# Performance work log

Measured on AMD Instinct MI355X. Metric: run time of the kernel, lower is better.

Reference implementation:

```python
import jax, jax.numpy as jnp
import numpy as np

N_NODES = 100000
N_EDGES = 1600000
HID = 128
N_CONV = 3  # num_layers - 1
OUT_DIM = 1
BN_EPS = 1e-5


def _batchnorm(z, gamma, beta):
    # training-mode BN over node dim (batch statistics, biased variance)
    mean = jnp.mean(z, axis=0)
    var = jnp.mean((z - mean) ** 2, axis=0)
    return (z - mean) * jax.lax.rsqrt(var + BN_EPS) * gamma + beta


def setup_inputs() -> dict:
    key = jax.random.key(0)
    ks = jax.random.split(key, 16)
    s = 0.05
    inp = {
        "x": jax.random.randint(ks[0], (N_NODES,), 0, 2, dtype=jnp.int32),
        "edge_index": jax.random.randint(ks[1], (2, N_EDGES), 0, N_NODES, dtype=jnp.int64),
        "emb": jax.random.normal(ks[2], (2, HID), jnp.float32) * s,
        "W1": jax.random.normal(ks[3], (N_CONV, HID, HID), jnp.float32) * s,
        "W2": jax.random.normal(ks[4], (N_CONV, HID, HID), jnp.float32) * s,
        "bn1_g": jnp.ones((N_CONV, HID), jnp.float32),
        "bn1_b": jnp.zeros((N_CONV, HID), jnp.float32),
        "bn2_g": jnp.ones((N_CONV, HID), jnp.float32),
        "bn2_b": jnp.zeros((N_CONV, HID), jnp.float32),
        "rW1": jax.random.normal(ks[5], (4 * HID, HID), jnp.float32) * s,
        "rb1": jnp.zeros((HID,), jnp.float32),
        "rW2": jax.random.normal(ks[6], (HID, OUT_DIM), jnp.float32) * s,
        "rb2": jnp.zeros((OUT_DIM,), jnp.float32),
    }
    return inp


def reference(x, edge_index, emb, W1, W2, bn1_g, bn1_b, bn2_g, bn2_b, rW1, rb1, rW2, rb2):
    n = x.shape[0]
    src, dst = edge_index[0], edge_index[1]
    h = emb[x]  # [N, HID]
    reps = [h]
    for i in range(N_CONV):
        # GINConv: mlp((1+eps)*h + sum_{j in N(i)} h_j), eps=0
        agg = jax.ops.segment_sum(h[src], dst, num_segments=n)
        z = h + agg
        z = jnp.einsum('nd,df->nf', z, W1[i])
        z = jax.nn.relu(_batchnorm(z, bn1_g[i], bn1_b[i]))
        z = jnp.einsum('nd,df->nf', z, W2[i])
        z = _batchnorm(z, bn2_g[i], bn2_b[i])  # PyG BatchNorm after conv
        h = jax.nn.elu(z)
        reps.append(h)
    cat = jnp.concatenate(reps, axis=-1)  # [N, 4*HID]
    hid = jax.nn.relu(cat @ rW1 + rb1)
    return hid @ rW2 + rb2  # [N, OUT_DIM]
```

## Files before the change

### kernel.cpp

```cpp
#include <hip/hip_runtime.h>
#include <hip/hip_fp16.h>
#include <cstdint>
#include <cstddef>

#define NN 100000
#define NE 1600000
#define HID 128
#define BN_EPS 1e-5f
#define NB_SCAN 98
#define BM 96
#define NBLK ((NN + BM - 1) / BM)
#define NBC  ((NN + 255) / 256)
#define SA 72
#define SC_CHUNKS 256
#define SC_RANGE (NN / 8)
#define SC_EPC (NE / SC_CHUNKS)

typedef __attribute__((ext_vector_type(8))) short bf16x8;
typedef __attribute__((ext_vector_type(4))) float f32x4;
typedef __attribute__((ext_vector_type(4))) unsigned short u16x4;

static constexpr size_t SZ_NODE = (size_t)NN * HID * 4;
static constexpr size_t SZ_H16  = (size_t)NN * HID * 2;
static constexpr size_t OFF_P   = 0;
static constexpr size_t OFF_Q   = SZ_NODE;
static constexpr size_t OFF_R   = 2 * SZ_NODE;
static constexpr size_t OFF_CSR = 3 * SZ_NODE;
static constexpr size_t OFF_RP  = OFF_CSR + (size_t)NE * 4;
static constexpr size_t OFF_ZZ  = ((OFF_RP + (size_t)(NN + 1) * 4 + 255) / 256) * 256;
static constexpr size_t OFF_CNT = OFF_ZZ;
static constexpr size_t OFF_BS  = OFF_CNT + (((size_t)NN * 4 + 255) / 256) * 256;
static constexpr size_t OFF_FLG = OFF_BS + 512;
static constexpr size_t OFF_SS  = OFF_FLG + 256;
static constexpr size_t OFF_SCT = OFF_SS + 5 * 256 * 4;
static constexpr size_t ZZ_END  = ((OFF_SCT + 5 * 4 + 255) / 256) * 256;
static constexpr size_t ZZ_BYTES = ZZ_END - OFF_ZZ;
static constexpr size_t OFF_AC  = ZZ_END;
static constexpr size_t OFF_E   = OFF_AC + 6 * 256 * 4;
static constexpr size_t OFF_WSP = OFF_E + 512 * 4;
static constexpr size_t WS_NEEDED = OFF_WSP + (size_t)8 * 2 * HID * HID * 2;

__device__ __forceinline__ unsigned short f2bf(float f) {
  unsigned u = __float_as_uint(f);
  unsigned r = (u + 0x7fffu + ((u >> 16) & 1u)) >> 16;
  return (unsigned short)r;
}
__device__ __forceinline__ float bf2f(unsigned short b) {
  return __uint_as_float(((unsigned)b) << 16);
}
__device__ __forceinline__ int edge_at(const int* __restrict__ E, int f, int idx) {
  return f ? E[2 * (long long)idx] : E[idx];
}

__global__ void k_detect(const int* __restrict__ E, int* __restrict__ flag) {
  if (threadIdx.x == 0 && blockIdx.x == 0) {
    int f = 1;
    for (int i = 1; i < 256; i += 2)
      if (E[i] != 0) { f = 0; break; }
    *flag = f;
  }
}

__global__ __launch_bounds__(256) void k_hist(const int* __restrict__ E,
                                              const int* __restrict__ flag,
                                              int* __restrict__ cnt) {
  const int f = *flag;
  for (int e = blockIdx.x * blockDim.x + threadIdx.x; e < NE;
       e += gridDim.x * blockDim.x) {
    int d = edge_at(E, f, NE + e);
    d = min(max(d, 0), NN - 1);
    atomicAdd(&cnt[d], 1);
  }
}

__global__ __launch_bounds__(256) void k_scan1(const int* __restrict__ cnt,
                                               int* __restrict__ rp,
                                               int* __restrict__ bs) {
  __shared__ int s[256];
  const int tid = threadIdx.x;
  const int base = blockIdx.x * 1024 + tid * 4;
  int v0 = 0, v1 = 0, v2 = 0, v3 = 0;
  if (base + 0 < NN) v0 = cnt[base + 0];
  if (base + 1 < NN) v1 = cnt[base + 1];
  if (base + 2 < NN) v2 = cnt[base + 2];
  if (base + 3 < NN) v3 = cnt[base + 3];
  const int t0 = v0, t1 = t0 + v1, t2 = t1 + v2, t3 = t2 + v3;
  s[tid] = t3;
  __syncthreads();
  for (int off = 1; off < 256; off <<= 1) {
    int xv = 0;
    if (tid >= off) xv = s[tid - off];
    __syncthreads();
    if (tid >= off) s[tid] += xv;
    __syncthreads();
  }
  const int excl = tid ? s[tid - 1] : 0;
  if (base + 0 < NN) rp[base + 0] = excl;
  if (base + 1 < NN) rp[base + 1] = excl + t0;
  if (base + 2 < NN) rp[base + 2] = excl + t1;
  if (base + 3 < NN) rp[base + 3] = excl + t2;
  if (tid == 255) bs[blockIdx.x] = s[255];
}

__global__ __launch_bounds__(128) void k_scan2(int* __restrict__ bs) {
  __shared__ int s[128];
  const int tid = threadIdx.x;
  s[tid] = (tid < NB_SCAN) ? bs[tid] : 0;
  __syncthreads();
  for (int off = 1; off < 128; off <<= 1) {
    int xv = 0;
    if (tid >= off) xv = s[tid - off];
    __syncthreads();
    if (tid >= off) s[tid] += xv;
    __syncthreads();
  }
  if (tid < NB_SCAN) bs[tid] = tid ? s[tid - 1] : 0;
}

__global__ __launch_bounds__(256) void k_scan3(int* __restrict__ rp,
                                               const int* __restrict__ bs,
                                               int* __restrict__ cursor) {
  const int off = bs[blockIdx.x];
  const int base = blockIdx.x * 1024 + threadIdx.x * 4;
  #pragma unroll
  for (int j = 0; j < 4; ++j) {
    const int i = base + j;
    if (i < NN) {
      const int v = rp[i] + off;
      rp[i] = v;
      cursor[i] = v;
    }
  }
  if (blockIdx.x == 0 && threadIdx.x == 0) rp[NN] = NE;
}

__global__ __launch_bounds__(256) void k_scatter(const int* __restrict__ E,
                                                 const int* __restrict__ flag,
                                                 int* __restrict__ cursor,
                                                 int* __restrict__ csr) {
  const int f = *flag;
  const int r = blockIdx.x & 7;
  const int chunk = blockIdx.x >> 3;
  const int lo = r * SC_RANGE, hi = lo + SC_RANGE;
  const int ebeg = chunk * SC_EPC, eend = ebeg + SC_EPC;
  for (int e = ebeg + threadIdx.x; e < eend; e += 256) {
    int d = edge_at(E, f, NE + e);
    d = min(max(d, 0), NN - 1);
    if (d >= lo && d < hi) {
      int s = edge_at(E, f, e);
      s = min(max(s, 0), NN - 1);
      const int pos = atomicAdd(&cursor[d], 1);
      if ((unsigned)pos < (unsigned)NE) csr[pos] = s;
    }
  }
}

__global__ __launch_bounds__(256) void k_prepw(const float* __restrict__ W1,
                                               const float* __restrict__ W2,
                                               const float* __restrict__ rW1,
                                               short* __restrict__ wsp) {
  const int g = blockIdx.x * 256 + threadIdx.x;
  const int m = g >> 14, idx = g & 16383;
  const int k = idx >> 7, n = idx & 127;
  const float* src;
  switch (m) {
    case 0: src = W2; break;
    case 1: src = W1 + 1 * HID * HID; break;
    case 2: src = W2 + 1 * HID * HID; break;
    case 3: src = W1 + 2 * HID * HID; break;
    case 4: src = W2 + 2 * HID * HID; break;
    case 5: src = rW1 + 1 * HID * HID; break;
    case 6: src = rW1 + 2 * HID * HID; break;
    default: src = rW1 + 3 * HID * HID; break;
  }
  const float v = src[k * HID + n];
  const unsigned short hb = f2bf(v);
  short* dst = wsp + (size_t)m * 32768;
  dst[n * HID + k] = (short)hb;
  dst[16384 + n * HID + k] = (short)f2bf(v - bf2f(hb));
}

__global__ __launch_bounds__(256) void k_prep(const float* __restrict__ emb,
                                              const float* __restrict__ W1,
                                              const float* __restrict__ rW1,
                                              float* __restrict__ ee) {
  const int t = threadIdx.x;
  const int f = t & 127;
  const float* er = emb + (t >> 7) * HID;
  float se = 0.f, sr = 0.f;
  for (int k = 0; k < HID; ++k) {
    const float ev = er[k];
    se = fmaf(ev, W1[k * HID + f], se);
    sr = fmaf(ev, rW1[k * HID + f], sr);
  }
  ee[t] = se;
  ee[256 + t] = sr;
}

__global__ __launch_bounds__(256) void k_cnt(const int* __restrict__ x,
                                             const int* __restrict__ rp,
                                             const int* __restrict__ csr,
                                             int* __restrict__ a01,
                                             float* __restrict__ momp) {
  const int n = blockIdx.x * 256 + threadIdx.x;
  float m[5] = {0.f, 0.f, 0.f, 0.f, 0.f};
  if (n < NN) {
    const int beg = rp[n], end = rp[n + 1];
    int c1 = 0;
    for (int j = beg; j < end; ++j) c1 += x[csr[j]] & 1;
    const int a1 = c1 + (x[n] & 1);
    const int a0 = (end - beg + 1) - a1;
    a01[n] = a0 | (a1 << 16);
    m[0] = (float)a0;
    m[1] = (float)a1;
    m[2] = (float)a0 * (float)a0;
    m[3] = (float)a1 * (float)a1;
    m[4] = (float)a0 * (float)a1;
  }
  #pragma unroll
  for (int j = 0; j < 5; ++j)
    #pragma unroll
    for (int off = 1; off < 64; off <<= 1) m[j] += __shfl_xor(m[j], off);
  __shared__ float sm[5][4];
  const int lane = threadIdx.x & 63, wv = threadIdx.x >> 6;
  if (lane == 0)
    #pragma unroll
    for (int j = 0; j < 5; ++j) sm[j][wv] = m[j];
  __syncthreads();
  if (threadIdx.x == 0)
    #pragma unroll
    for (int j = 0; j < 5; ++j)
      momp[j * NBC + blockIdx.x] = sm[j][0] + sm[j][1] + sm[j][2] + sm[j][3];
}

__global__ __launch_bounds__(128) void k_bnmom(const float* __restrict__ momp,
                                               const float* __restrict__ ee,
                                               const float* __restrict__ g,
                                               const float* __restrict__ b,
                                               float* __restrict__ a,
                                               float* __restrict__ c) {
  __shared__ float red[5][128];
  const int t = threadIdx.x;
  float s[5] = {0.f, 0.f, 0.f, 0.f, 0.f};
  for (int i = t; i < NBC; i += 128)
    #pragma unroll
    for (int j = 0; j < 5; ++j) s[j] += momp[j * NBC + i];
  #pragma unroll
  for (int j = 0; j < 5; ++j) red[j][t] = s[j];
  __syncthreads();
  for (int off = 64; off; off >>= 1) {
    if (t < off)
      #pragma unroll
      for (int j = 0; j < 5; ++j) red[j][t] += red[j][t + off];
    __syncthreads();
  }
  const float S0 = red[0][0], S1 = red[1][0];
  const float S00 = red[2][0], S11 = red[3][0], S01 = red[4][0];
  const float inv_n = 1.0f / (float)NN;
  const float e0 = ee[t], e1 = ee[128 + t];
  const float mean = (S0 * e0 + S1 * e1) * inv_n;
  const float msq = (S00 * e0 * e0 + 2.f * S01 * e0 * e1 + S11 * e1 * e1) * inv_n;
  float var = fmaxf(msq - mean * mean, 0.f);
  const float rs = rsqrtf(var + BN_EPS);
  const float av = g[t] * rs;
  a[t] = av;
  c[t] = b[t] - mean * av;
}

__global__ __launch_bounds__(256) void k_l1expand(const int* __restrict__ a01,
                                                  const float* __restrict__ ee,
                                                  float* __restrict__ u1) {
  const int total = NN * 32;
  for (int i = blockIdx.x * blockDim.x + threadIdx.x; i < total;
       i += gridDim.x * blockDim.x) {
    const int node = i >> 5, q = i & 31;
    const int p = a01[node];
    const float a0 = (float)(p & 0xffff), a1 = (float)(p >> 16);
    const float4 e0q = ((const float4*)ee)[q];
    const float4 e1q = ((const float4*)ee)[32 + q];
    float4 u;
    u.x = a0 * e0q.x + a1 * e1q.x;
    u.y = a0 * e0q.y + a1 * e1q.y;
    u.z = a0 * e0q.z + a1 * e1q.z;
    u.w = a0 * e0q.w + a1 * e1q.w;
    ((float4*)(u1 + (size_t)node * HID))[q] = u;
  }
}

__global__ __launch_bounds__(256) void k_agg(const __half* __restrict__ h,
                                             const int* __restrict__ rp,
                                             const int* __restrict__ csr,
                                             float* __restrict__ z) {
  const int wid = blockIdx.x * 4 + (threadIdx.x >> 6);
  const int lane = threadIdx.x & 63;
  if (wid >= NN) return;
  const int beg = rp[wid], end = rp[wid + 1];
  float2 acc = __half22float2(*((const __half2*)(h + (size_t)wid * HID) + lane));
  for (int j = beg; j < end; j += 64) {
    const int cnt = min(64, end - j);
    int idx = (lane < cnt) ? csr[j + lane] : 0;
    idx = min(max(idx, 0), NN - 1);
    int k = 0;
    for (; k + 4 <= cnt; k += 4) {
      const int s0 = __shfl(idx, k + 0), s1 = __shfl(idx, k + 1);
      const int s2 = __shfl(idx, k + 2), s3 = __shfl(idx, k + 3);
      const float2 v0 = __half22float2(*((const __half2*)(h + (size_t)s0 * HID) + lane));
      const float2 v1 = __half22float2(*((const __half2*)(h + (size_t)s1 * HID) + lane));
      const float2 v2 = __half22float2(*((const __half2*)(h + (size_t)s2 * HID) + lane));
      const float2 v3 = __half22float2(*((const __half2*)(h + (size_t)s3 * HID) + lane));
      acc.x += (v0.x + v1.x) + (v2.x + v3.x);
      acc.y += (v0.y + v1.y) + (v2.y + v3.y);
    }
    for (; k < cnt; ++k) {
      const int s = __shfl(idx, k);
      const float2 v = __half22float2(*((const __half2*)(h + (size_t)s * HID) + lane));
      acc.x += v.x;
      acc.y += v.y;
    }
  }
  *(float2*)(z + (size_t)wid * HID + lane * 2) = acc;
}

template <int IN_ACT, int OUT_MODE>
__global__ __launch_bounds__(256, 2) void k_gemm(
    float* A, const short* __restrict__ Wsp,
    const float* __restrict__ ina, const float* __restrict__ inc,
    float* __restrict__ out, float* __restrict__ part) {
  __shared__ short Ah[BM * SA];
  __shared__ short Al[BM * SA];
  __shared__ short Wh[HID * SA];
  __shared__ short Wl[HID * SA];
  const int tid = threadIdx.x;
  const int lane = tid & 63, wv = tid >> 6;
  const int tq = lane >> 4, tl = lane & 15;
  const int wc = wv * 32;
  const int m0 = blockIdx.x * BM;

  f32x4 acc[6][2];
  #pragma unroll
  for (int i = 0; i < 6; ++i)
    #pragma unroll
    for (int j = 0; j < 2; ++j) acc[i][j] = (f32x4)(0.f);

  for (int kt = 0; kt < HID; kt += 64) {
    if (kt) __syncthreads();
    #pragma unroll
    for (int p = 0; p < 6; ++p) {
      const int flat = p * 256 + tid;
      const int m = flat >> 4, kq = flat & 15;
      const int gm = m0 + m, gk = kt + kq * 4;
      float vv[4] = {0.f, 0.f, 0.f, 0.f};
      if (gm < NN) {
        const float4 v = *(const float4*)(A + (size_t)gm * HID + gk);
        vv[0] = v.x; vv[1] = v.y; vv[2] = v.z; vv[3] = v.w;
        if (IN_ACT == 1) {
          const float4 a4 = *(const float4*)(ina + gk);
          const float4 c4 = *(const float4*)(inc + gk);
          vv[0] = fmaxf(fmaf(vv[0], a4.x, c4.x), 0.f);
          vv[1] = fmaxf(fmaf(vv[1], a4.y, c4.y), 0.f);
          vv[2] = fmaxf(fmaf(vv[2], a4.z, c4.z), 0.f);
          vv[3] = fmaxf(fmaf(vv[3], a4.w, c4.w), 0.f);
        }
      }
      u16x4 hh, ll;
      #pragma unroll
      for (int j = 0; j < 4; ++j) {
        const unsigned short hb = f2bf(vv[j]);
        hh[j] = hb;
        ll[j] = f2bf(vv[j] - bf2f(hb));
      }
      *(u16x4*)(&Ah[m * SA + kq * 4]) = hh;
      *(u16x4*)(&Al[m * SA + kq * 4]) = ll;
    }
    #pragma unroll
    for (int p = 0; p < 8; ++p) {
      const int flat = p * 256 + tid;
      const int n = flat >> 4, kq = flat & 15;
      const u16x4 hh = *(const u16x4*)(Wsp + n * HID + kt + kq * 4);
      const u16x4 ll = *(const u16x4*)(Wsp + 16384 + n * HID + kt + kq * 4);
      *(u16x4*)(&Wh[n * SA + kq * 4]) = hh;
      *(u16x4*)(&Wl[n * SA + kq * 4]) = ll;
    }
    __syncthreads();
    #pragma unroll
    for (int kc = 0; kc < 64; kc += 32) {
      const int ko = kc + tq * 8;
      bf16x8 wh[2], wl[2];
      #pragma unroll
      for (int fn = 0; fn < 2; ++fn) {
        const int c = (wc + fn * 16 + tl) * SA + ko;
        wh[fn] = *(const bf16x8*)(&Wh[c]);
        wl[fn] = *(const bf16x8*)(&Wl[c]);
      }
      #pragma unroll
      for (int fm = 0; fm < 6; ++fm) {
        const int r = (fm * 16 + tl) * SA + ko;
        const bf16x8 ah = *(const bf16x8*)(&Ah[r]);
        const bf16x8 al = *(const bf16x8*)(&Al[r]);
        #pragma unroll
        for (int fn = 0; fn < 2; ++fn) {
          acc[fm][fn] = __builtin_amdgcn_mfma_f32_16x16x32_bf16(ah, wh[fn], acc[fm][fn], 0, 0, 0);
          acc[fm][fn] = __builtin_amdgcn_mfma_f32_16x16x32_bf16(ah, wl[fn], acc[fm][fn], 0, 0, 0);
          acc[fm][fn] = __builtin_amdgcn_mfma_f32_16x16x32_bf16(al, wh[fn], acc[fm][fn], 0, 0, 0);
        }
      }
    }
  }

  #pragma unroll
  for (int fm = 0; fm < 6; ++fm) {
    #pragma unroll
    for (int reg = 0; reg < 4; ++reg) {
      const int row = m0 + fm * 16 + tq * 4 + reg;
      if (row < NN) {
        float* op = out + (size_t)row * HID + wc + tl;
        op[0] = acc[fm][0][reg];
        op[16] = acc[fm][1][reg];
      }
    }
  }
  if (OUT_MODE == 0) {
    #pragma unroll
    for (int fn = 0; fn < 2; ++fn) {
      float s = 0.f, q = 0.f;
      #pragma unroll
      for (int fm = 0; fm < 6; ++fm)
        #pragma unroll
        for (int reg = 0; reg < 4; ++reg) {
          const float v = acc[fm][fn][reg];
          s += v;
          q = fmaf(v, v, q);
        }
      s += __shfl_xor(s, 16); q += __shfl_xor(q, 16);
      s += __shfl_xor(s, 32); q += __shfl_xor(q, 32);
      if (lane < 16) {
        const int col = wc + fn * 16 + lane;
        part[(size_t)blockIdx.x * 256 + col] = s;
        part[(size_t)blockIdx.x * 256 + 128 + col] = q;
      }
    }
  }
}

__global__ __launch_bounds__(256, 2) void k_rdgemm(
    const __half* __restrict__ h1, const __half* __restrict__ h2,
    const __half* __restrict__ h3, const short* __restrict__ wsp,
    const int* __restrict__ x, const float* __restrict__ ee,
    const float* __restrict__ rb1, const float* __restrict__ rW2,
    const float* __restrict__ rb2, float* __restrict__ out) {
  __shared__ short Ah[BM * SA];
  __shared__ short Al[BM * SA];
  __shared__ short Wh[HID * SA];
  __shared__ short Wl[HID * SA];
  const int tid = threadIdx.x;
  const int lane = tid & 63, wv = tid >> 6;
  const int tq = lane >> 4, tl = lane & 15;
  const int wc = wv * 32;
  const int m0 = blockIdx.x * BM;

  f32x4 acc[6][2];
  #pragma unroll
  for (int i = 0; i < 6; ++i)
    #pragma unroll
    for (int j = 0; j < 2; ++j) acc[i][j] = (f32x4)(0.f);

  for (int t6 = 0; t6 < 6; ++t6) {
    const __half* hsrc = (t6 < 2) ? h1 : (t6 < 4) ? h2 : h3;
    const short* Ws = wsp + (size_t)(t6 >> 1) * 32768;
    const int kt = (t6 & 1) * 64;
    if (t6) __syncthreads();
    #pragma unroll
    for (int p = 0; p < 6; ++p) {
      const int flat = p * 256 + tid;
      const int m = flat >> 4, kq = flat & 15;
      const int gm = m0 + m, gk = kt + kq * 4;
      float vv[4] = {0.f, 0.f, 0.f, 0.f};
      if (gm < NN) {
        const __half2 x0 = *(const __half2*)(hsrc + (size_t)gm * HID + gk);
        const __half2 x1 = *(const __half2*)(hsrc + (size_t)gm * HID + gk + 2);
        const float2 f0 = __half22float2(x0);
        const float2 f1 = __half22float2(x1);
        vv[0] = f0.x; vv[1] = f0.y; vv[2] = f1.x; vv[3] = f1.y;
      }
      u16x4 hh, ll;
      #pragma unroll
      for (int j = 0; j < 4; ++j) {
        const unsigned short hb = f2bf(vv[j]);
        hh[j] = hb;
        ll[j] = f2bf(vv[j] - bf2f(hb));
      }
      *(u16x4*)(&Ah[m * SA + kq * 4]) = hh;
      *(u16x4*)(&Al[m * SA + kq * 4]) = ll;
    }
    #pragma unroll
    for (int p = 0; p < 8; ++p) {
      const int flat = p * 256 + tid;
      const int n = flat >> 4, kq = flat & 15;
      const u16x4 hh = *(const u16x4*)(Ws + n * HID + kt + kq * 4);
      const u16x4 ll = *(const u16x4*)(Ws + 16384 + n * HID + kt + kq * 4);
      *(u16x4*)(&Wh[n * SA + kq * 4]) = hh;
      *(u16x4*)(&Wl[n * SA + kq * 4]) = ll;
    }
    __syncthreads();
    #pragma unroll
    for (int kc = 0; kc < 64; kc += 32) {
      const int ko = kc + tq * 8;
      bf16x8 wh[2], wl[2];
      #pragma unroll
      for (int fn = 0; fn < 2; ++fn) {
        const int c = (wc + fn * 16 + tl) * SA + ko;
        wh[fn] = *(const bf16x8*)(&Wh[c]);
        wl[fn] = *(const bf16x8*)(&Wl[c]);
      }
      #pragma unroll
      for (int fm = 0; fm < 6; ++fm) {
        const int r = (fm * 16 + tl) * SA + ko;
        const bf16x8 ah = *(const bf16x8*)(&Ah[r]);
        const bf16x8 al = *(const bf16x8*)(&Al[r]);
        #pragma unroll
        for (int fn = 0; fn < 2; ++fn) {
          acc[fm][fn] = __builtin_amdgcn_mfma_f32_16x16x32_bf16(ah, wh[fn], acc[fm][fn], 0, 0, 0);
          acc[fm][fn] = __builtin_amdgcn_mfma_f32_16x16x32_bf16(ah, wl[fn], acc[fm][fn], 0, 0, 0);
          acc[fm][fn] = __builtin_amdgcn_mfma_f32_16x16x32_bf16(al, wh[fn], acc[fm][fn], 0, 0, 0);
        }
      }
    }
  }

  const int c0 = wc + tl, c1 = wc + 16 + tl;
  const float rb_0 = rb1[c0], rb_1 = rb1[c1];
  const float w2_0 = rW2[c0], w2_1 = rW2[c1];
  const float r0_0 = ee[256 + c0], r0_1 = ee[256 + c1];
  const float r1_0 = ee[384 + c0], r1_1 = ee[384 + c1];
  __syncthreads();
  float* rs = (float*)Ah;
  #pragma unroll
  for (int fm = 0; fm < 6; ++fm) {
    #pragma unroll
    for (int reg = 0; reg < 4; ++reg) {
      const int row = fm * 16 + tq * 4 + reg;
      const int grow = m0 + row;
      const int xv = (grow < NN) ? (x[grow] & 1) : 0;
      const float g0 = acc[fm][0][reg] + rb_0 + (xv ? r1_0 : r0_0);
      const float g1 = acc[fm][1][reg] + rb_1 + (xv ? r1_1 : r0_1);
      float p = fmaxf(g0, 0.f) * w2_0 + fmaxf(g1, 0.f) * w2_1;
      p += __shfl_xor(p, 1);
      p += __shfl_xor(p, 2);
      p += __shfl_xor(p, 4);
      p += __shfl_xor(p, 8);
      if (tl == 0) rs[row * 4 + wv] = p;
    }
  }
  __syncthreads();
  if (tid < BM) {
    const int grow = m0 + tid;
    if (grow < NN)
      out[grow] = rs[tid * 4 + 0] + rs[tid * 4 + 1] + rs[tid * 4 + 2] +
                  rs[tid * 4 + 3] + rb2[0];
  }
}

__global__ __launch_bounds__(256) void k_bnstat(const float* __restrict__ part,
                                                const float* __restrict__ g,
                                                const float* __restrict__ b,
                                                float* __restrict__ a,
                                                float* __restrict__ c,
                                                float* __restrict__ S,
                                                int* __restrict__ ctr) {
  const int tid = threadIdx.x;
  float acc = 0.f;
  for (int r = blockIdx.x; r < NBLK; r += 64) acc += part[(size_t)r * 256 + tid];
  atomicAdd(&S[tid], acc);
  __syncthreads();
  __threadfence();
  __shared__ int last;
  if (tid == 0) last = (atomicAdd(ctr, 1) == 63);
  __syncthreads();
  if (!last) return;
  __threadfence();
  const float tot = atomicAdd(&S[tid], 0.f);
  __shared__ float sm[256];
  sm[tid] = tot;
  __syncthreads();
  if (tid < 128) {
    const float inv_n = 1.0f / (float)NN;
    const float mean = sm[tid] * inv_n;
    float var = fmaxf(sm[tid + 128] * inv_n - mean * mean, 0.f);
    const float rs = rsqrtf(var + BN_EPS);
    const float av = g[tid] * rs;
    a[tid] = av;
    c[tid] = b[tid] - mean * av;
  }
}

__global__ __launch_bounds__(256) void k_act(const float* __restrict__ v,
                                             const float* __restrict__ a,
                                             const float* __restrict__ c,
                                             __half* __restrict__ h) {
  const int total = NN * 32;
  for (int i = blockIdx.x * blockDim.x + threadIdx.x; i < total;
       i += gridDim.x * blockDim.x) {
    const int node = i >> 5, q = i & 31;
    const float4 vv = *(const float4*)(v + (size_t)node * HID + q * 4);
    const float4 a4 = ((const float4*)a)[q];
    const float4 c4 = ((const float4*)c)[q];
    float z;
    float o0, o1, o2, o3;
    z = fmaf(vv.x, a4.x, c4.x); o0 = z > 0.f ? z : expm1f(z);
    z = fmaf(vv.y, a4.y, c4.y); o1 = z > 0.f ? z : expm1f(z);
    z = fmaf(vv.z, a4.z, c4.z); o2 = z > 0.f ? z : expm1f(z);
    z = fmaf(vv.w, a4.w, c4.w); o3 = z > 0.f ? z : expm1f(z);
    const __half2 p0 = __floats2half2_rn(o0, o1);
    const __half2 p1 = __floats2half2_rn(o2, o3);
    uint2 u;
    u.x = *reinterpret_cast<const unsigned*>(&p0);
    u.y = *reinterpret_cast<const unsigned*>(&p1);
    *(uint2*)(h + (size_t)node * HID + q * 4) = u;
  }
}

extern "C" void kernel_launch(void* const* d_in, const int* in_sizes, int n_in,
                              void* d_out, int out_size, void* d_ws,
                              size_t ws_size, hipStream_t stream) {
  if (ws_size < WS_NEEDED) return;

  const int* x = (const int*)d_in[0];
  const int* E = (const int*)d_in[1];
  const float* emb = (const float*)d_in[2];
  const float* W1 = (const float*)d_in[3];
  const float* W2 = (const float*)d_in[4];
  const float* bn1g = (const float*)d_in[5];
  const float* bn1b = (const float*)d_in[6];
  const float* bn2g = (const float*)d_in[7];
  const float* bn2b = (const float*)d_in[8];
  const float* rW1 = (const float*)d_in[9];
  const float* rb1 = (const float*)d_in[10];
  const float* rW2 = (const float*)d_in[11];
  const float* rb2 = (const float*)d_in[12];
  float* outp = (float*)d_out;

  char* ws = (char*)d_ws;
  float* P = (float*)(ws + OFF_P);
  float* Q = (float*)(ws + OFF_Q);
  float* R = (float*)(ws + OFF_R);
  int* csr = (int*)(ws + OFF_CSR);
  int* rp = (int*)(ws + OFF_RP);
  int* cnt = (int*)(ws + OFF_CNT);
  int* bs = (int*)(ws + OFF_BS);
  int* flag = (int*)(ws + OFF_FLG);
  float* SS = (float*)(ws + OFF_SS);
  int* SCT = (int*)(ws + OFF_SCT);
  float* ac = (float*)(ws + OFF_AC);
  float* ee = (float*)(ws + OFF_E);
  short* wsp = (short*)(ws + OFF_WSP);
  __half* h1 = (__half*)P;
  __half* h2 = (__half*)((char*)P + SZ_H16);
  __half* h3 = (__half*)R;
  float* part = R;
  int* a01 = (int*)((char*)P + (4 << 20));
  float* momp = (float*)((char*)P + (8 << 20));

  hipMemsetAsync(ws + OFF_ZZ, 0, ZZ_BYTES, stream);
  k_detect<<<1, 64, 0, stream>>>(E, flag);
  k_hist<<<2048, 256, 0, stream>>>(E, flag, cnt);
  k_scan1<<<NB_SCAN, 256, 0, stream>>>(cnt, rp, bs);
  k_scan2<<<1, 128, 0, stream>>>(bs);
  k_scan3<<<NB_SCAN, 256, 0, stream>>>(rp, bs, cnt);
  k_scatter<<<SC_CHUNKS * 8, 256, 0, stream>>>(E, flag, cnt, csr);
  k_prep<<<1, 256, 0, stream>>>(emb, W1, rW1, ee);
  k_prepw<<<512, 256, 0, stream>>>(W1, W2, rW1, wsp);

  float* a1 = ac + 0 * 256, *c1 = a1 + HID;
  float* a2 = ac + 1 * 256, *c2 = a2 + HID;

  k_cnt<<<NBC, 256, 0, stream>>>(x, rp, csr, a01, momp);
  k_bnmom<<<1, 128, 0, stream>>>(momp, ee, bn1g, bn1b, a1, c1);
  k_l1expand<<<2048, 256, 0, stream>>>(a01, ee, Q);
  k_gemm<1, 0><<<NBLK, 256, 0, stream>>>(Q, wsp + 0 * 32768, a1, c1, Q, part);
  k_bnstat<<<64, 256, 0, stream>>>(part, bn2g, bn2b, a2, c2, SS + 0 * 256, SCT + 0);
  k_act<<<2048, 256, 0, stream>>>(Q, a2, c2, h1);

  int inst = 1;
  for (int i = 1; i < 3; ++i) {
    float* b1a = ac + (2 * i) * 256, *b1c = b1a + HID;
    float* b2a = ac + (2 * i + 1) * 256, *b2c = b2a + HID;
    const int s1 = (i == 1) ? 1 : 3;
    const __half* hin = (i == 1) ? h1 : h2;
    k_agg<<<NN / 4, 256, 0, stream>>>(hin, rp, csr, Q);
    k_gemm<0, 0><<<NBLK, 256, 0, stream>>>(Q, wsp + (size_t)s1 * 32768,
                                           nullptr, nullptr, Q, part);
    k_bnstat<<<64, 256, 0, stream>>>(part, bn1g + i * HID, bn1b + i * HID, b1a,
                                     b1c, SS + inst * 256, SCT + inst);
    ++inst;
    k_gemm<1, 0><<<NBLK, 256, 0, stream>>>(Q, wsp + (size_t)(s1 + 1) * 32768,
                                           b1a, b1c, Q, part);
    k_bnstat<<<64, 256, 0, stream>>>(part, bn2g + i * HID, bn2b + i * HID, b2a,
                                     b2c, SS + inst * 256, SCT + inst);
    ++inst;
    k_act<<<2048, 256, 0, stream>>>(Q, b2a, b2c, (i == 1) ? h2 : h3);
  }

  k_rdgemm<<<NBLK, 256, 0, stream>>>(h1, h2, h3, wsp + (size_t)5 * 32768, x, ee,
                                     rb1, rW2, rb2, outp);
}
```

Measured before the change: 738.6 us.

## Load GEMM weight fragments from global and range-partition histogram atomics

Both GEMM kernels stop staging the split-bf16 weights in shared memory. Each wave now reads its weight fragments directly from global memory (through the cache), and launch bounds rise from 2 to 4 blocks per CU, trading LDS traffic and capacity for higher occupancy. The histogram kernel is restructured like the scatter kernel: each block handles one edge chunk and counts only destinations in one of 8 node ranges, to localize atomics. That multiplies edge reads by 8 in exchange for less atomic contention.

After: 719.5 us. -2.6%, faster.

```diff
diff --git a/kernel.cpp b/kernel.cpp
--- a/kernel.cpp
+++ b/kernel.cpp
@@ -65,11 +65,14 @@
                                               const int* __restrict__ flag,
                                               int* __restrict__ cnt) {
   const int f = *flag;
-  for (int e = blockIdx.x * blockDim.x + threadIdx.x; e < NE;
-       e += gridDim.x * blockDim.x) {
+  const int r = blockIdx.x & 7;
+  const int chunk = blockIdx.x >> 3;
+  const int lo = r * SC_RANGE, hi = lo + SC_RANGE;
+  const int ebeg = chunk * SC_EPC, eend = ebeg + SC_EPC;
+  for (int e = ebeg + threadIdx.x; e < eend; e += 256) {
     int d = edge_at(E, f, NE + e);
     d = min(max(d, 0), NN - 1);
-    atomicAdd(&cnt[d], 1);
+    if (d >= lo && d < hi) atomicAdd(&cnt[d], 1);
   }
 }
 
@@ -322,14 +325,12 @@
 }
 
 template <int IN_ACT, int OUT_MODE>
-__global__ __launch_bounds__(256, 2) void k_gemm(
+__global__ __launch_bounds__(256, 4) void k_gemm(
     float* A, const short* __restrict__ Wsp,
     const float* __restrict__ ina, const float* __restrict__ inc,
     float* __restrict__ out, float* __restrict__ part) {
   __shared__ short Ah[BM * SA];
   __shared__ short Al[BM * SA];
-  __shared__ short Wh[HID * SA];
-  __shared__ short Wl[HID * SA];
   const int tid = threadIdx.x;
   const int lane = tid & 63, wv = tid >> 6;
   const int tq = lane >> 4, tl = lane & 15;
@@ -372,29 +373,21 @@
       *(u16x4*)(&Ah[m * SA + kq * 4]) = hh;
       *(u16x4*)(&Al[m * SA + kq * 4]) = ll;
     }
-    #pragma unroll
-    for (int p = 0; p < 8; ++p) {
-      const int flat = p * 256 + tid;
-      const int n = flat >> 4, kq = flat & 15;
-      const u16x4 hh = *(const u16x4*)(Wsp + n * HID + kt + kq * 4);
-      const u16x4 ll = *(const u16x4*)(Wsp + 16384 + n * HID + kt + kq * 4);
-      *(u16x4*)(&Wh[n * SA + kq * 4]) = hh;
-      *(u16x4*)(&Wl[n * SA + kq * 4]) = ll;
-    }
     __syncthreads();
     #pragma unroll
     for (int kc = 0; kc < 64; kc += 32) {
-      const int ko = kc + tq * 8;
+      const int lo = kc + tq * 8;
+      const int go = kt + lo;
       bf16x8 wh[2], wl[2];
       #pragma unroll
       for (int fn = 0; fn < 2; ++fn) {
-        const int c = (wc + fn * 16 + tl) * SA + ko;
-        wh[fn] = *(const bf16x8*)(&Wh[c]);
-        wl[fn] = *(const bf16x8*)(&Wl[c]);
+        const int n = wc + fn * 16 + tl;
+        wh[fn] = *(const bf16x8*)(Wsp + n * HID + go);
+        wl[fn] = *(const bf16x8*)(Wsp + 16384 + n * HID + go);
       }
       #pragma unroll
       for (int fm = 0; fm < 6; ++fm) {
-        const int r = (fm * 16 + tl) * SA + ko;
+        const int r = (fm * 16 + tl) * SA + lo;
         const bf16x8 ah = *(const bf16x8*)(&Ah[r]);
         const bf16x8 al = *(const bf16x8*)(&Al[r]);
         #pragma unroll
@@ -442,7 +435,7 @@
   }
 }
 
-__global__ __launch_bounds__(256, 2) void k_rdgemm(
+__global__ __launch_bounds__(256, 4) void k_rdgemm(
     const __half* __restrict__ h1, const __half* __restrict__ h2,
     const __half* __restrict__ h3, const short* __restrict__ wsp,
     const int* __restrict__ x, const float* __restrict__ ee,
@@ -450,8 +443,6 @@
     const float* __restrict__ rb2, float* __restrict__ out) {
   __shared__ short Ah[BM * SA];
   __shared__ short Al[BM * SA];
-  __shared__ short Wh[HID * SA];
-  __shared__ short Wl[HID * SA];
   const int tid = threadIdx.x;
   const int lane = tid & 63, wv = tid >> 6;
   const int tq = lane >> 4, tl = lane & 15;
@@ -492,29 +483,21 @@
       *(u16x4*)(&Ah[m * SA + kq * 4]) = hh;
       *(u16x4*)(&Al[m * SA + kq * 4]) = ll;
     }
-    #pragma unroll
-    for (int p = 0; p < 8; ++p) {
-      const int flat = p * 256 + tid;
-      const int n = flat >> 4, kq = flat & 15;
-      const u16x4 hh = *(const u16x4*)(Ws + n * HID + kt + kq * 4);
-      const u16x4 ll = *(const u16x4*)(Ws + 16384 + n * HID + kt + kq * 4);
-      *(u16x4*)(&Wh[n * SA + kq * 4]) = hh;
-      *(u16x4*)(&Wl[n * SA + kq * 4]) = ll;
-    }
     __syncthreads();
     #pragma unroll
     for (int kc = 0; kc < 64; kc += 32) {
-      const int ko = kc + tq * 8;
+      const int lo = kc + tq * 8;
+      const int go = kt + lo;
       bf16x8 wh[2], wl[2];
       #pragma unroll
       for (int fn = 0; fn < 2; ++fn) {
-        const int c = (wc + fn * 16 + tl) * SA + ko;
-        wh[fn] = *(const bf16x8*)(&Wh[c]);
-        wl[fn] = *(const bf16x8*)(&Wl[c]);
+        const int n = wc + fn * 16 + tl;
+        wh[fn] = *(const bf16x8*)(Ws + n * HID + go);
+        wl[fn] = *(const bf16x8*)(Ws + 16384 + n * HID + go);
       }
       #pragma unroll
       for (int fm = 0; fm < 6; ++fm) {
-        const int r = (fm * 16 + tl) * SA + ko;
+        const int r = (fm * 16 + tl) * SA + lo;
         const bf16x8 ah = *(const bf16x8*)(&Ah[r]);
         const bf16x8 al = *(const bf16x8*)(&Al[r]);
         #pragma unroll
@@ -662,7 +645,7 @@
 
   hipMemsetAsync(ws + OFF_ZZ, 0, ZZ_BYTES, stream);
   k_detect<<<1, 64, 0, stream>>>(E, flag);
-  k_hist<<<2048, 256, 0, stream>>>(E, flag, cnt);
+  k_hist<<<SC_CHUNKS * 8, 256, 0, stream>>>(E, flag, cnt);
   k_scan1<<<NB_SCAN, 256, 0, stream>>>(cnt, rp, bs);
   k_scan2<<<1, 128, 0, stream>>>(bs);
   k_scan3<<<NB_SCAN, 256, 0, stream>>>(rp, bs, cnt);
```
